# Optimization experiments

Hardware: AMD Instinct MI355X
Metric: run time of the kernel (lower is better)

Reference implementation:

```python
import jax, jax.numpy as jnp
import numpy as np

B, C_ENC, H, W = 8, 512, 96, 96
N_SAMP = 64            # num_samples in forward
N_NODES = 2 * N_SAMP   # 64 pos + 64 neg per image
D = 256                # node feature dim after head_in_ln
N_HEADS = 8
DH = D // N_HEADS
SINKHORN_ITERS = 10


def _ln(x):
    # LayerNorm(elementwise_affine=False)
    m = x.mean(-1, keepdims=True)
    v = x.var(-1, keepdims=True)
    return (x - m) / jnp.sqrt(v + 1e-5)


def setup_inputs() -> dict:
    key = jax.random.key(0)
    ks = jax.random.split(key, 12)
    std = 0.01  # matches nn.init.normal_(std=0.01) in _init_weights
    inp = {
        "feat_s": jax.random.normal(ks[0], (B, C_ENC, H, W), jnp.float32),
        "score_s": jax.random.normal(ks[1], (B, 1, H, W), jnp.float32),
        "feat_t": jax.random.normal(ks[2], (B, C_ENC, H, W), jnp.float32),
        "score_t": jax.random.normal(ks[3], (B, 1, H, W), jnp.float32),
        "head_W1": std * jax.random.normal(ks[4], (C_ENC, D), jnp.float32),
        "head_b1": jnp.zeros((D,), jnp.float32),
        "head_W2": std * jax.random.normal(ks[5], (D, D), jnp.float32),
        "head_b2": jnp.zeros((D,), jnp.float32),
        "intra_W": jax.random.normal(ks[6], (4, D, D), jnp.float32) / jnp.sqrt(jnp.float32(D)),
        "intra_b": jnp.zeros((4, D), jnp.float32),
        "cross_W": jax.random.normal(ks[7], (4, D, D), jnp.float32) / jnp.sqrt(jnp.float32(D)),
        "cross_b": jnp.zeros((4, D), jnp.float32),
        "cls_W1": std * jax.random.normal(ks[8], (D, 128), jnp.float32),
        "cls_b1": jnp.zeros((128,), jnp.float32),
        "cls_W2": std * jax.random.normal(ks[9], (128, 1), jnp.float32),
        "cls_b2": jnp.zeros((1,), jnp.float32),
        "aff_A": jax.random.normal(ks[10], (D, D), jnp.float32) / jnp.sqrt(jnp.float32(D)),
    }
    return inp


def _sample_points(feat, score):
    # torch version: boolean-mask nonzero + random gather of 64 pos / 64 neg spatial
    # locations per image. JIT-friendly deterministic equivalent: top-64 highest
    # sigmoid scores = positives, top-64 lowest = negatives.
    s = jax.nn.sigmoid(score[:, 0].reshape(B, -1))            # [B, H*W]
    _, pos_idx = jax.lax.top_k(s, N_SAMP)
    _, neg_idx = jax.lax.top_k(-s, N_SAMP)
    idx = jnp.concatenate([pos_idx, neg_idx], axis=1)         # [B, 128]
    ff = feat.reshape(B, C_ENC, -1)                           # [B, 512, H*W]
    nodes = jnp.take_along_axis(ff, idx[:, None, :], axis=2)  # [B, 512, 128]
    nodes = nodes.transpose(0, 2, 1)                          # [B, 128, 512]
    labels = jnp.concatenate(
        [jnp.ones((B, N_SAMP, 1), feat.dtype), jnp.zeros((B, N_SAMP, 1), feat.dtype)], axis=1)
    return nodes, labels


def _mha(xq, xkv, Wp, bp):
    # standard multi-head attention (MultiHeadAttentionWrapper)
    q = xq @ Wp[0] + bp[0]
    k = xkv @ Wp[1] + bp[1]
    v = xkv @ Wp[2] + bp[2]
    sh = lambda t: t.reshape(t.shape[0], t.shape[1], N_HEADS, DH)
    att = jnp.einsum("bqhd,bkhd->bhqk", sh(q), sh(k)) / jnp.sqrt(jnp.float32(DH))
    att = jax.nn.softmax(att, axis=-1)
    o = jnp.einsum("bhqk,bkhd->bqhd", att, sh(v)).reshape(xq.shape[0], xq.shape[1], D)
    return o @ Wp[3] + bp[3], att.mean(1)


def _forward(feat_s, score_s, feat_t, score_t, head_W1, head_b1, head_W2, head_b2,
             intra_W, intra_b, cross_W, cross_b, cls_W1, cls_b1, cls_W2, cls_b2, aff_A):
    n1, l1 = _sample_points(feat_s, score_s)
    n2, l2 = _sample_points(feat_t, score_t)

    # head_in_ln: Linear -> LN -> ReLU -> Linear -> LN
    head = lambda x: _ln(jax.nn.relu(_ln(x @ head_W1 + head_b1)) @ head_W2 + head_b2)
    n1, n2 = head(n1), head(n2)

    # intra-domain graph (self-attention), shared weights for both domains
    n1, _ = _mha(n1, n1, intra_W, intra_b)
    n2, _ = _mha(n2, n2, intra_W, intra_b)

    # cross-domain graph (cross-attention both directions, shared weights)
    c1, _ = _mha(n1, n2, cross_W, cross_b)
    c2, _ = _mha(n2, n1, cross_W, cross_b)
    n1, n2 = c1, c2

    # node classification loss (BCEWithLogits, mean)
    cls = lambda x: jax.nn.relu(x @ cls_W1 + cls_b1) @ cls_W2 + cls_b2
    def bce_logits(logit, lab):
        return jnp.mean(jnp.maximum(logit, 0) - logit * lab + jnp.log1p(jnp.exp(-jnp.abs(logit))))
    node_loss = bce_logits(cls(n1), l1) + bce_logits(cls(n2), l2)

    # affinity + InstanceNorm2d(1) + sinkhorn refine
    Mmat = jnp.einsum("bnd,de,bme->bnm", n1, aff_A, n2)       # [B, 128, 128]
    mu = Mmat.mean((1, 2), keepdims=True)
    var = Mmat.var((1, 2), keepdims=True)
    K = (Mmat - mu) / jnp.sqrt(var + 1e-5)
    for _ in range(SINKHORN_ITERS):  # log-space row/col normalization
        K = K - jax.nn.logsumexp(K, axis=2, keepdims=True)
        K = K - jax.nn.logsumexp(K, axis=1, keepdims=True)
    P = jnp.exp(K)

    # matching loss = BCEFocalLoss(gamma=2, alpha=0.25) vs label-agreement matrix
    gt = (l1[:, :, 0][:, :, None] == l2[:, :, 0][:, None, :]).astype(P.dtype)
    pt = jnp.clip(P, 1e-6, 1.0 - 1e-6)
    mat_loss = jnp.mean(-0.25 * (1 - pt) ** 2 * gt * jnp.log(pt)
                        - 0.75 * pt ** 2 * (1 - gt) * jnp.log(1 - pt))

    total_loss = node_loss + 10.0 * mat_loss
    return n1, total_loss


def reference(feat_s, score_s, feat_t, score_t, head_W1, head_b1, head_W2, head_b2,
              intra_W, intra_b, cross_W, cross_b, cls_W1, cls_b1, cls_W2, cls_b2, aff_A):
    return _forward(feat_s, score_s, feat_t, score_t, head_W1, head_b1, head_W2, head_b2,
                    intra_W, intra_b, cross_W, cross_b, cls_W1, cls_b1, cls_W2, cls_b2, aff_A)
```

## Files before the change

### kernel.cpp

```cpp
#include <hip/hip_runtime.h>
#include <math.h>

#define BIMG 8
#define HW 9216
#define CENC 512
#define NN 128
#define DD 256
#define NHEAD 8
#define DH 32
#define ROWS1 1024
#define ROWS2 2048
#define TAILB 520

typedef unsigned long long ull;
typedef unsigned short u16;
typedef __attribute__((ext_vector_type(4))) float f32x4;
typedef __attribute__((ext_vector_type(4))) unsigned u32x4;
typedef __attribute__((ext_vector_type(2))) unsigned u32x2;

__device__ __forceinline__ u16 f2bf(float f) {
  unsigned u = __float_as_uint(f);
  u += 0x7fffu + ((u >> 16) & 1u);
  return (u16)(u >> 16);
}
__device__ __forceinline__ float bf2f(unsigned h) { return __uint_as_float(h << 16); }
__device__ __forceinline__ unsigned pack2(float a, float b) {
  return (unsigned)f2bf(a) | ((unsigned)f2bf(b) << 16);
}
__device__ __forceinline__ void mfma_b(f32x4& acc, u32x4 a, u32x4 b) {
  asm volatile("v_mfma_f32_16x16x32_bf16 %0, %1, %2, %0" : "+v"(acc) : "v"(a), "v"(b));
}

__device__ __forceinline__ ull cmpex_keep(ull k, ull o, bool keepMax) {
  return ((k > o) == keepMax) ? k : o;
}
__device__ __forceinline__ void bsort64(ull& k, int lane) {
#pragma unroll
  for (int size = 2; size <= 64; size <<= 1) {
#pragma unroll
    for (int stride = size >> 1; stride > 0; stride >>= 1) {
      ull o = __shfl_xor(k, stride);
      bool keepMax = (((lane & size) == 0) == ((lane & stride) == 0));
      k = cmpex_keep(k, o, keepMax);
    }
  }
}
__device__ __forceinline__ void bmerge64(ull& top, ull b, int lane) {
  ull rev = __shfl_xor(b, 63);
  ull m = top > rev ? top : rev;
#pragma unroll
  for (int stride = 32; stride > 0; stride >>= 1) {
    ull o = __shfl_xor(m, stride);
    m = cmpex_keep(m, o, (lane & stride) == 0);
  }
  top = m;
}
__device__ __forceinline__ ull lds_merge(ull a, ull brev, int lane) {
  ull m = a > brev ? a : brev;
#pragma unroll
  for (int stride = 32; stride > 0; stride >>= 1) {
    ull o = __shfl_xor(m, stride);
    m = cmpex_keep(m, o, (lane & stride) == 0);
  }
  return m;
}

__global__ __launch_bounds__(512) void head_kernel(const float* __restrict__ score_s,
                                                   const float* __restrict__ score_t,
                                                   int* __restrict__ idx_out,
                                                   float* __restrict__ loss_acc,
                                                   const float* __restrict__ hw1,
                                                   const float* __restrict__ hw2,
                                                   const float* __restrict__ iw,
                                                   const float* __restrict__ cw,
                                                   const float* __restrict__ aw,
                                                   const float* __restrict__ clsW1,
                                                   const float* __restrict__ intra_b,
                                                   const float* __restrict__ cross_b,
                                                   u16* __restrict__ wt,
                                                   u16* __restrict__ w1t,
                                                   u16* __restrict__ wt_f,
                                                   float* __restrict__ bfq) {
  __shared__ union {
    struct { ull sm[512]; float tile[32][33]; } a;
    struct { float Wo[32][264]; float Wc[256][40]; } b;
  } HS;
  int tid = threadIdx.x;
  if (blockIdx.x < 32) {
    int blk = blockIdx.x;
    int bi = blk >> 1, neg = blk & 1;
    int lane = tid & 63, w = tid >> 6;
    if (blk == 0 && tid < 4) loss_acc[tid] = 0.f;
    const float* sp = (bi < 8 ? score_s : score_t) + (size_t)(bi & 7) * HW;
    int q0 = w * 18;
    ull keys[18];
#pragma unroll
    for (int j = 0; j < 18; ++j) {
      float x = sp[(q0 + j) * 64 + lane];
      unsigned ub = __float_as_uint(x);
      unsigned u = (ub & 0x80000000u) ? ~ub : (ub | 0x80000000u);
      if (neg) u = ~u;
      int gi = (q0 + j) * 64 + lane;
      keys[j] = ((ull)u << 32) | (unsigned)(~gi);
    }
    ull top1 = keys[0]; bsort64(top1, lane);
    ull top2 = keys[9]; bsort64(top2, lane);
#pragma unroll
    for (int j = 1; j < 9; ++j) {
      ull k1 = keys[j], k2 = keys[9 + j];
      bsort64(k1, lane);
      bsort64(k2, lane);
      bmerge64(top1, k1, lane);
      bmerge64(top2, k2, lane);
    }
    bmerge64(top1, top2, lane);
    HS.a.sm[w * 64 + lane] = top1;
    __syncthreads();
    if (w < 4) {
      ull m = lds_merge(HS.a.sm[(2 * w) * 64 + lane],
                        HS.a.sm[(2 * w + 1) * 64 + (63 - lane)], lane);
      HS.a.sm[(2 * w) * 64 + lane] = m;
    }
    __syncthreads();
    if (w < 2) {
      ull m = lds_merge(HS.a.sm[(4 * w) * 64 + lane],
                        HS.a.sm[(4 * w + 2) * 64 + (63 - lane)], lane);
      HS.a.sm[(4 * w) * 64 + lane] = m;
    }
    __syncthreads();
    if (w == 0) {
      ull m = lds_merge(HS.a.sm[lane], HS.a.sm[4 * 64 + (63 - lane)], lane);
      idx_out[bi * NN + neg * 64 + lane] = (int)(~(unsigned)(m & 0xffffffffull));
    }
  } else if (blockIdx.x < 800) {
    int bid = blockIdx.x - 32;
    const float* src; u16* dst; int K, k0, n0;
    if (bid < 128) {
      src = hw1; dst = wt; K = 512;
      k0 = (bid >> 3) * 32; n0 = (bid & 7) * 32;
    } else {
      int id2 = bid - 128;
      int m = id2 >> 6, tt = id2 & 63;
      K = 256;
      k0 = (tt >> 3) * 32; n0 = (tt & 7) * 32;
      src = (m == 0) ? hw2 : (m < 5) ? iw + (size_t)(m - 1) * 65536
          : (m < 9) ? cw + (size_t)(m - 5) * 65536 : aw;
      dst = wt + 131072 + (size_t)m * 65536;
    }
    int r = tid >> 3, c = (tid & 7) * 4;
    if (tid < 256) {
      float4 v = *(const float4*)&src[(size_t)(k0 + r) * 256 + n0 + c];
      HS.a.tile[r][c] = v.x; HS.a.tile[r][c + 1] = v.y;
      HS.a.tile[r][c + 2] = v.z; HS.a.tile[r][c + 3] = v.w;
    }
    __syncthreads();
    if (tid < 256) {
      u32x2 o;
      o[0] = pack2(HS.a.tile[c][r], HS.a.tile[c + 1][r]);
      o[1] = pack2(HS.a.tile[c + 2][r], HS.a.tile[c + 3][r]);
      *(u32x2*)&dst[(size_t)(n0 + r) * K + k0 + c] = o;
    }
  } else if (blockIdx.x < 832) {
    int bid3 = blockIdx.x - 800;
    int k0 = (bid3 >> 2) * 32, n0 = (bid3 & 3) * 32;
    int r = tid >> 3, c = (tid & 7) * 4;
    if (tid < 256) {
      float4 v = *(const float4*)&clsW1[(size_t)(k0 + r) * 128 + n0 + c];
      HS.a.tile[r][c] = v.x; HS.a.tile[r][c + 1] = v.y;
      HS.a.tile[r][c + 2] = v.z; HS.a.tile[r][c + 3] = v.w;
    }
    __syncthreads();
    if (tid < 256) {
      u32x2 o;
      o[0] = pack2(HS.a.tile[c][r], HS.a.tile[c + 1][r]);
      o[1] = pack2(HS.a.tile[c + 2][r], HS.a.tile[c + 3][r]);
      *(u32x2*)&w1t[(size_t)(n0 + r) * 256 + k0 + c] = o;
    }
  } else {
    int bid4 = blockIdx.x - 832;
    int z = bid4 >> 6, tt = bid4 & 63;
    int k0 = (tt >> 3) * 32, n0 = (tt & 7) * 32;
    const float* Wo = iw + 3 * 65536;
    const float* Wc = cw + (size_t)z * 65536;
    for (int e = tid; e < 2048; e += 512) {
      int row = e >> 6, c4 = (e & 63) * 4;
      *(float4*)&HS.b.Wo[row][c4] = *(const float4*)&Wo[(size_t)(k0 + row) * 256 + c4];
    }
    for (int e = tid; e < 2048; e += 512) {
      int row = e >> 3, c4 = (e & 7) * 4;
      *(float4*)&HS.b.Wc[row][c4] = *(const float4*)&Wc[(size_t)row * 256 + n0 + c4];
    }
    __syncthreads();
    int k = tid >> 4, half = (tid >> 3) & 1, nb = (tid & 7) * 4;
    float a0 = 0.f, a1 = 0.f, a2 = 0.f, a3 = 0.f;
    int jb = half * 128;
#pragma unroll 8
    for (int j = 0; j < 128; ++j) {
      float wo = HS.b.Wo[k][jb + j];
      float4 wc = *(const float4*)&HS.b.Wc[jb + j][nb];
      a0 += wo * wc.x; a1 += wo * wc.y; a2 += wo * wc.z; a3 += wo * wc.w;
    }
    a0 += __shfl_xor(a0, 8); a1 += __shfl_xor(a1, 8);
    a2 += __shfl_xor(a2, 8); a3 += __shfl_xor(a3, 8);
    if (half == 0) {
      u16* dst = wt_f + (size_t)z * 65536;
      dst[(size_t)(n0 + nb + 0) * 256 + k0 + k] = f2bf(a0);
      dst[(size_t)(n0 + nb + 1) * 256 + k0 + k] = f2bf(a1);
      dst[(size_t)(n0 + nb + 2) * 256 + k0 + k] = f2bf(a2);
      dst[(size_t)(n0 + nb + 3) * 256 + k0 + k] = f2bf(a3);
    }
    if (k0 == 0 && tid < 32) {
      float b = 0.f;
      const float* bo = intra_b + 768;
      for (int j = 0; j < 256; ++j) b += bo[j] * HS.b.Wc[j][tid];
      bfq[z * 256 + n0 + tid] = b + cross_b[z * 256 + n0 + tid];
    }
  }
}

__global__ __launch_bounds__(512) void gemm1_fused(const float* __restrict__ feat_s,
                                                   const float* __restrict__ feat_t,
                                                   const int* __restrict__ idxb,
                                                   const u16* __restrict__ wt_h1,
                                                   const float* __restrict__ head_b1,
                                                   u16* __restrict__ bufA,
                                                   float* __restrict__ st1) {
  __shared__ u16 As[16][520];
  __shared__ u16 Bs[256][40];
  int t = threadIdx.x, l = t & 63, w = t >> 6;
  int m0 = blockIdx.x * 16;
#pragma unroll
  for (int row = 0; row < 16; ++row) {
    int grow = m0 + row;
    int bi = grow >> 7, n = grow & 127, b = bi & 7;
    const float* fp = (bi < 8) ? feat_s : feat_t;
    int pos = idxb[bi * NN + n];
    As[row][t] = f2bf(fp[(size_t)b * CENC * HW + (size_t)t * HW + pos]);
  }
  __syncthreads();
  f32x4 acc[2];
  acc[0] = (f32x4){0.f, 0.f, 0.f, 0.f};
  acc[1] = (f32x4){0.f, 0.f, 0.f, 0.f};
  for (int kc = 0; kc < 16; ++kc) {
#pragma unroll
    for (int i = 0; i < 2; ++i) {
      int e = t + i * 512;
      int nn2 = e >> 2, ch8 = (e & 3) * 8;
      *(u32x4*)&Bs[nn2][ch8] = *(const u32x4*)&wt_h1[(size_t)nn2 * 512 + kc * 32 + ch8];
    }
    __syncthreads();
    u32x4 af = *(const u32x4*)&As[l & 15][kc * 32 + (l >> 4) * 8];
#pragma unroll
    for (int i = 0; i < 2; ++i) {
      u32x4 bf = *(const u32x4*)&Bs[w * 32 + i * 16 + (l & 15)][(l >> 4) * 8];
      mfma_b(acc[i], af, bf);
    }
    __syncthreads();
  }
  asm volatile("s_nop 7\n\ts_nop 7" ::);
  int rbase = m0 + (l >> 4) * 4;
#pragma unroll
  for (int i = 0; i < 2; ++i) {
    int col = w * 32 + i * 16 + (l & 15);
    float bb = head_b1[col];
#pragma unroll
    for (int r = 0; r < 4; ++r) {
      int row = rbase + r;
      float o = acc[i][r] + bb;
      bufA[(size_t)row * 256 + col] = f2bf(o);
      float s = o, q = o * o;
#pragma unroll
      for (int m = 1; m < 16; m <<= 1) { s += __shfl_xor(s, m); q += __shfl_xor(q, m); }
      if ((l & 15) == 0) {
        st1[(size_t)row * 32 + w * 2 + i]      = s;
        st1[(size_t)row * 32 + 16 + w * 2 + i] = q;
      }
    }
  }
}

template<int K>
__global__ __launch_bounds__(512) void gemm_mf(const u16* __restrict__ A,
                                               const u16* __restrict__ Wt,
                                               const float* __restrict__ bias,
                                               u16* __restrict__ Cb,
                                               float* __restrict__ Cf,
                                               int ldc,
                                               const float* __restrict__ in_stats, int in_relu,
                                               float* __restrict__ out_stats,
                                               int Wz, int Cbz, int bz) {
  constexpr int LDK = K + 8;
  constexpr int KC = K / 8;
  __shared__ u16 As[32][LDK];
  __shared__ u16 Bs[64][LDK];
  __shared__ float mS[32], rS[32];
  int z = blockIdx.z;
  Wt += (size_t)z * Wz;
  if (Cb)   Cb += (size_t)z * Cbz;
  if (bias) bias += (size_t)z * bz;
  int n0 = blockIdx.x * 64, m0 = blockIdx.y * 32;
  int t = threadIdx.x;
  if (in_stats) {
    if (t < 32) {
      const float* sp = in_stats + (size_t)(m0 + t) * 32;
      float s = 0.f, q = 0.f;
#pragma unroll
      for (int i = 0; i < 16; ++i) { s += sp[i]; q += sp[16 + i]; }
      float mm = s * (1.f / 256.f);
      float var = q * (1.f / 256.f) - mm * mm;
      mS[t] = mm;
      rS[t] = rsqrtf(fmaxf(var, 0.f) + 1e-5f);
    }
    __syncthreads();
  }
  for (int i = t; i < 32 * KC; i += 512) {
    int row = i / KC, c8 = (i % KC) * 8;
    u32x4 av = *(const u32x4*)&A[(size_t)(m0 + row) * K + c8];
    if (in_stats) {
      float mm = mS[row], rr = rS[row];
#pragma unroll
      for (int j = 0; j < 4; ++j) {
        float f0 = (bf2f(av[j] & 0xffffu) - mm) * rr;
        float f1 = (bf2f(av[j] >> 16) - mm) * rr;
        if (in_relu) { f0 = fmaxf(f0, 0.f); f1 = fmaxf(f1, 0.f); }
        av[j] = pack2(f0, f1);
      }
    }
    *(u32x4*)&As[row][c8] = av;
  }
  for (int i = t; i < 64 * KC; i += 512) {
    int row = i / KC, c8 = (i % KC) * 8;
    *(u32x4*)&Bs[row][c8] = *(const u32x4*)&Wt[(size_t)(n0 + row) * K + c8];
  }
  __syncthreads();
  int l = t & 63, w = t >> 6;
  int wr = w >> 2, wc = w & 3;
  int fra = wr * 16 + (l & 15);
  int frk = (l >> 4) * 8;
  int fb = wc * 16 + (l & 15);
  f32x4 acc = {0.f, 0.f, 0.f, 0.f};
#pragma unroll
  for (int ks = 0; ks < K / 32; ++ks) {
    u32x4 af = *(const u32x4*)&As[fra][ks * 32 + frk];
    u32x4 bf = *(const u32x4*)&Bs[fb][ks * 32 + frk];
    mfma_b(acc, af, bf);
  }
  asm volatile("s_nop 7\n\ts_nop 7" ::);
  int col0 = n0 + wc * 16 + (l & 15);
  int rbase = m0 + wr * 16 + (l >> 4) * 4;
  float b0 = bias ? bias[col0] : 0.f;
#pragma unroll
  for (int r = 0; r < 4; ++r) {
    int row = rbase + r;
    float o0 = acc[r] + b0;
    if (Cb) Cb[(size_t)row * 256 + col0] = f2bf(o0);
    if (Cf && row < ROWS1) Cf[(size_t)row * ldc + col0] = o0;
    if (out_stats) {
      float s0 = o0, q0 = o0 * o0;
#pragma unroll
      for (int m = 1; m < 16; m <<= 1) { s0 += __shfl_xor(s0, m); q0 += __shfl_xor(q0, m); }
      if ((l & 15) == 0) {
        int slot = (n0 >> 4) + wc;
        out_stats[(size_t)row * 32 + slot]      = s0;
        out_stats[(size_t)row * 32 + 16 + slot] = q0;
      }
    }
  }
}

__global__ __launch_bounds__(256) void attn_kernel(const u16* __restrict__ q,
                                                   const u16* __restrict__ k,
                                                   const u16* __restrict__ v,
                                                   u16* __restrict__ o, int swap) {
  __shared__ __align__(16) float Ks[NN][DH];
  __shared__ __align__(16) float Vs[NN][DH];
  __shared__ __align__(16) float Ex[64][3][34];
  int blk = blockIdx.x;
  int bb = blk >> 4, h = (blk >> 1) & 7, qh = blk & 1;
  int kb = swap ? (bb ^ 8) : bb;
  int t = threadIdx.x;
  int rr = t & 63, part = t >> 6;
  for (int e = t; e < 1024; e += 256) {
    int which = e >> 9;
    int idx2 = e & 511;
    int r = idx2 >> 2, c8 = (idx2 & 3) * 8;
    u32x4 val = *(const u32x4*)&(which ? v : k)[(size_t)(kb * NN + r) * DD + h * DH + c8];
    float* dst = which ? &Vs[r][c8] : &Ks[r][c8];
#pragma unroll
    for (int i = 0; i < 4; ++i) {
      dst[2 * i]     = bf2f(val[i] & 0xffffu);
      dst[2 * i + 1] = bf2f(val[i] >> 16);
    }
  }
  __syncthreads();
  int qrow = bb * NN + qh * 64 + rr;
  float4 q4[8];
  {
    const u16* qp = q + (size_t)qrow * DD + h * DH;
#pragma unroll
    for (int c4 = 0; c4 < 4; ++c4) {
      u32x4 u = *(const u32x4*)&qp[c4 * 8];
      q4[c4 * 2].x = bf2f(u[0] & 0xffffu); q4[c4 * 2].y = bf2f(u[0] >> 16);
      q4[c4 * 2].z = bf2f(u[1] & 0xffffu); q4[c4 * 2].w = bf2f(u[1] >> 16);
      q4[c4 * 2 + 1].x = bf2f(u[2] & 0xffffu); q4[c4 * 2 + 1].y = bf2f(u[2] >> 16);
      q4[c4 * 2 + 1].z = bf2f(u[3] & 0xffffu); q4[c4 * 2 + 1].w = bf2f(u[3] >> 16);
    }
  }
  const float scale = 0.17677669529663687f;
  int j0 = part * 32;
  float mx = -1e30f;
  for (int j = j0; j < j0 + 32; ++j) {
    const float4* kp = (const float4*)Ks[j];
    float s = 0.f;
#pragma unroll
    for (int c4 = 0; c4 < 8; ++c4) {
      float4 kv = kp[c4];
      s += q4[c4].x * kv.x + q4[c4].y * kv.y + q4[c4].z * kv.z + q4[c4].w * kv.w;
    }
    mx = fmaxf(mx, s * scale);
  }
  float acc[DH];
#pragma unroll
  for (int c = 0; c < DH; ++c) acc[c] = 0.f;
  float den = 0.f;
  for (int j = j0; j < j0 + 32; ++j) {
    const float4* kp = (const float4*)Ks[j];
    float s = 0.f;
#pragma unroll
    for (int c4 = 0; c4 < 8; ++c4) {
      float4 kv = kp[c4];
      s += q4[c4].x * kv.x + q4[c4].y * kv.y + q4[c4].z * kv.z + q4[c4].w * kv.w;
    }
    float e = __expf(s * scale - mx);
    den += e;
    const float4* vp = (const float4*)Vs[j];
#pragma unroll
    for (int c4 = 0; c4 < 8; ++c4) {
      float4 vv = vp[c4];
      acc[c4 * 4 + 0] += e * vv.x; acc[c4 * 4 + 1] += e * vv.y;
      acc[c4 * 4 + 2] += e * vv.z; acc[c4 * 4 + 3] += e * vv.w;
    }
  }
  if (part) {
#pragma unroll
    for (int c = 0; c < DH; ++c) Ex[rr][part - 1][c] = acc[c];
    Ex[rr][part - 1][32] = mx;
    Ex[rr][part - 1][33] = den;
  }
  __syncthreads();
  if (part == 0) {
    float M = mx;
#pragma unroll
    for (int p = 0; p < 3; ++p) M = fmaxf(M, Ex[rr][p][32]);
    float f0 = __expf(mx - M);
    float fp[3];
    float dt = den * f0;
#pragma unroll
    for (int p = 0; p < 3; ++p) { fp[p] = __expf(Ex[rr][p][32] - M); dt += Ex[rr][p][33] * fp[p]; }
    float inv = 1.0f / dt;
    unsigned ovu[16];
#pragma unroll
    for (int c = 0; c < 16; ++c) {
      float x0 = acc[2 * c] * f0, x1 = acc[2 * c + 1] * f0;
#pragma unroll
      for (int p = 0; p < 3; ++p) { x0 += Ex[rr][p][2 * c] * fp[p]; x1 += Ex[rr][p][2 * c + 1] * fp[p]; }
      ovu[c] = pack2(x0 * inv, x1 * inv);
    }
    unsigned* op = (unsigned*)(o + (size_t)qrow * DD + h * DH);
#pragma unroll
    for (int i = 0; i < 4; ++i) {
      u32x4 w4;
      w4[0] = ovu[4 * i]; w4[1] = ovu[4 * i + 1]; w4[2] = ovu[4 * i + 2]; w4[3] = ovu[4 * i + 3];
      *(u32x4*)&op[4 * i] = w4;
    }
  }
}

struct SkSmem {
  union { u16 tmpL[128][264]; float Km[128][133]; } u;
  float u_[NN];
  float v_[NN];
  float red[20];
};
struct ClsSmem {
  float xs[4][256];
  float part[4][128];
  float red[8];
};
union TailSmem { SkSmem sk; ClsSmem cls; };

__device__ __forceinline__ void ticket_finalize(float* acc, float* out) {
  __threadfence();
  int tk = atomicAdd((int*)acc + 3, 1);
  if (tk == TAILB - 1) {
    float a0 = atomicAdd(acc + 0, 0.0f);
    float a1 = atomicAdd(acc + 1, 0.0f);
    out[ROWS1 * DD] = a0 + 10.0f * a1;
  }
}

__global__ __launch_bounds__(1024) void tail_kernel(const u16* __restrict__ bufH,
                                                    const u16* __restrict__ wt_af,
                                                    const u16* __restrict__ w1t,
                                                    const float* __restrict__ b1,
                                                    const float* __restrict__ W2,
                                                    const float* __restrict__ b2,
                                                    float* __restrict__ acc,
                                                    float* __restrict__ out) {
  __shared__ TailSmem sm;
  int t = threadIdx.x;
  int bid = blockIdx.x;
  if (bid < 8) {
    int b = bid;
    int l = t & 63, w = t >> 6;
    int tr = w >> 1;
    const u16* c1 = bufH + (size_t)(b * 128) * 256;
    const u16* c2 = bufH + (size_t)(1024 + b * 128) * 256;
    {
      int tcB = (w & 1) * 8;
      f32x4 accA[8];
#pragma unroll
      for (int i = 0; i < 8; ++i) accA[i] = (f32x4){0.f, 0.f, 0.f, 0.f};
      for (int ks = 0; ks < 8; ++ks) {
        int kk = ks * 32 + (l >> 4) * 8;
        u32x4 af = *(const u32x4*)&c1[(size_t)(tr * 16 + (l & 15)) * 256 + kk];
#pragma unroll
        for (int i = 0; i < 8; ++i) {
          u32x4 bf = *(const u32x4*)&wt_af[(size_t)((tcB + i) * 16 + (l & 15)) * 256 + kk];
          mfma_b(accA[i], af, bf);
        }
      }
      asm volatile("s_nop 7\n\ts_nop 7" ::);
      int rb = tr * 16 + (l >> 4) * 4;
#pragma unroll
      for (int i = 0; i < 8; ++i) {
        int col = (tcB + i) * 16 + (l & 15);
#pragma unroll
        for (int r2 = 0; r2 < 4; ++r2)
          sm.sk.u.tmpL[rb + r2][col] = f2bf(accA[i][r2]);
      }
    }
    __syncthreads();
    f32x4 aB[4];
    {
      int tcB = (w & 1) * 4;
#pragma unroll
      for (int i = 0; i < 4; ++i) aB[i] = (f32x4){0.f, 0.f, 0.f, 0.f};
      for (int ks = 0; ks < 8; ++ks) {
        int kk = ks * 32 + (l >> 4) * 8;
        u32x4 af = *(const u32x4*)&sm.sk.u.tmpL[tr * 16 + (l & 15)][kk];
#pragma unroll
        for (int i = 0; i < 4; ++i) {
          u32x4 bf = *(const u32x4*)&c2[(size_t)((tcB + i) * 16 + (l & 15)) * 256 + kk];
          mfma_b(aB[i], af, bf);
        }
      }
      asm volatile("s_nop 7\n\ts_nop 7" ::);
    }
    __syncthreads();
    {
      int tcB = (w & 1) * 4;
      int rb = tr * 16 + (l >> 4) * 4;
#pragma unroll
      for (int i = 0; i < 4; ++i) {
        int col = (tcB + i) * 16 + (l & 15);
#pragma unroll
        for (int r2 = 0; r2 < 4; ++r2)
          sm.sk.u.Km[rb + r2][col] = aB[i][r2];
      }
    }
    __syncthreads();
    int r = t >> 3, cg = t & 7;
    int c = t >> 3, rg = t & 7;
    float kr[16], kc[16];
    {
#pragma unroll
      for (int q4 = 0; q4 < 4; ++q4) {
        float4 f = *(const float4*)&sm.sk.u.Km[r][cg * 16 + q4 * 4];
        kr[q4 * 4 + 0] = f.x; kr[q4 * 4 + 1] = f.y; kr[q4 * 4 + 2] = f.z; kr[q4 * 4 + 3] = f.w;
      }
#pragma unroll
      for (int q = 0; q < 16; ++q)
        kc[q] = sm.sk.u.Km[rg * 16 + q][c];
    }
    float s = 0.f;
#pragma unroll
    for (int q = 0; q < 16; ++q) s += kr[q];
    for (int m = 1; m < 64; m <<= 1) s += __shfl_xor(s, m);
    if ((t & 63) == 0) sm.sk.red[t >> 6] = s;
    __syncthreads();
    if (t == 0) { float tt = 0.f; for (int i = 0; i < 16; ++i) tt += sm.sk.red[i]; sm.sk.red[16] = tt; }
    __syncthreads();
    float mu = sm.sk.red[16] * (1.0f / 16384.f);
    __syncthreads();
    float sq = 0.f;
#pragma unroll
    for (int q = 0; q < 16; ++q) { float d = kr[q] - mu; sq += d * d; }
    for (int m = 1; m < 64; m <<= 1) sq += __shfl_xor(sq, m);
    if ((t & 63) == 0) sm.sk.red[t >> 6] = sq;
    __syncthreads();
    if (t == 0) { float tt = 0.f; for (int i = 0; i < 16; ++i) tt += sm.sk.red[i]; sm.sk.red[17] = tt; }
    __syncthreads();
    float inv = 1.0f / sqrtf(sm.sk.red[17] * (1.0f / 16384.f) + 1e-5f);
#pragma unroll
    for (int q = 0; q < 16; ++q) { kr[q] = (kr[q] - mu) * inv; kc[q] = (kc[q] - mu) * inv; }
    if (t < NN) { sm.sk.u_[t] = 0.f; sm.sk.v_[t] = 0.f; }
    __syncthreads();
    for (int iter = 0; iter < 10; ++iter) {
      float tmp[16];
      {
        const float4* vp = (const float4*)(sm.sk.v_ + cg * 16);
#pragma unroll
        for (int q4 = 0; q4 < 4; ++q4) {
          float4 f = vp[q4];
          tmp[q4 * 4 + 0] = kr[q4 * 4 + 0] - f.x; tmp[q4 * 4 + 1] = kr[q4 * 4 + 1] - f.y;
          tmp[q4 * 4 + 2] = kr[q4 * 4 + 2] - f.z; tmp[q4 * 4 + 3] = kr[q4 * 4 + 3] - f.w;
        }
        float mx = tmp[0];
#pragma unroll
        for (int q = 1; q < 16; ++q) mx = fmaxf(mx, tmp[q]);
        for (int m = 1; m < 8; m <<= 1) mx = fmaxf(mx, __shfl_xor(mx, m));
        float smv = 0.f;
#pragma unroll
        for (int q = 0; q < 16; ++q) smv += __expf(tmp[q] - mx);
        for (int m = 1; m < 8; m <<= 1) smv += __shfl_xor(smv, m);
        if (cg == 0) sm.sk.u_[r] = mx + __logf(smv);
      }
      __syncthreads();
      {
        const float4* up = (const float4*)(sm.sk.u_ + rg * 16);
#pragma unroll
        for (int q4 = 0; q4 < 4; ++q4) {
          float4 f = up[q4];
          tmp[q4 * 4 + 0] = kc[q4 * 4 + 0] - f.x; tmp[q4 * 4 + 1] = kc[q4 * 4 + 1] - f.y;
          tmp[q4 * 4 + 2] = kc[q4 * 4 + 2] - f.z; tmp[q4 * 4 + 3] = kc[q4 * 4 + 3] - f.w;
        }
        float mx = tmp[0];
#pragma unroll
        for (int q = 1; q < 16; ++q) mx = fmaxf(mx, tmp[q]);
        for (int m = 1; m < 8; m <<= 1) mx = fmaxf(mx, __shfl_xor(mx, m));
        float smv = 0.f;
#pragma unroll
        for (int q = 0; q < 16; ++q) smv += __expf(tmp[q] - mx);
        for (int m = 1; m < 8; m <<= 1) smv += __shfl_xor(smv, m);
        if (rg == 0) sm.sk.v_[c] = mx + __logf(smv);
      }
      __syncthreads();
    }
    float ur = sm.sk.u_[r];
    float fsum = 0.f;
    {
      const float4* vp = (const float4*)(sm.sk.v_ + cg * 16);
#pragma unroll
      for (int q4 = 0; q4 < 4; ++q4) {
        float4 f = vp[q4];
        float vv[4] = {f.x, f.y, f.z, f.w};
#pragma unroll
        for (int j = 0; j < 4; ++j) {
          float P = __expf(kr[q4 * 4 + j] - ur - vv[j]);
          float pt = fminf(fmaxf(P, 1e-6f), 1.0f - 1e-6f);
          int col = cg * 16 + q4 * 4 + j;
          bool gt = (r < 64) == (col < 64);
          float wgt = gt ? (-0.25f * (1.f - pt) * (1.f - pt)) : (-0.75f * pt * pt);
          float lg = gt ? __logf(pt) : __logf(1.f - pt);
          fsum += wgt * lg;
        }
      }
    }
    for (int m = 1; m < 64; m <<= 1) fsum += __shfl_xor(fsum, m);
    if ((t & 63) == 0) sm.sk.red[t >> 6] = fsum;
    __syncthreads();
    if (t == 0) {
      float tt = 0.f; for (int i = 0; i < 16; ++i) tt += sm.sk.red[i];
      atomicAdd(acc + 1, tt * (1.0f / 131072.f));
      ticket_finalize(acc, out);
    }
  } else {
    int row0 = (bid - 8) * 4;
    {
      int rr = t >> 8, cc = t & 255;
      sm.cls.xs[rr][cc] = bf2f(bufH[(size_t)(row0 + rr) * 256 + cc]);
    }
    __syncthreads();
    int grp = t >> 8, col = t & 127, kh = (t >> 7) & 1;
    const u16* wp = w1t + (size_t)col * 256 + kh * 128;
    const float* xp = &sm.cls.xs[grp][kh * 128];
    float h = 0.f;
#pragma unroll
    for (int i = 0; i < 16; ++i) {
      u32x4 wv = *(const u32x4*)&wp[i * 8];
      const float* x8 = xp + i * 8;
      h += x8[0] * bf2f(wv[0] & 0xffffu) + x8[1] * bf2f(wv[0] >> 16)
         + x8[2] * bf2f(wv[1] & 0xffffu) + x8[3] * bf2f(wv[1] >> 16)
         + x8[4] * bf2f(wv[2] & 0xffffu) + x8[5] * bf2f(wv[2] >> 16)
         + x8[6] * bf2f(wv[3] & 0xffffu) + x8[7] * bf2f(wv[3] >> 16);
    }
    if (kh == 1) sm.cls.part[grp][col] = h;
    __syncthreads();
    if (kh == 0) {
      float z = h + sm.cls.part[grp][col] + b1[col];
      float p = fmaxf(z, 0.f) * W2[col];
#pragma unroll
      for (int m = 1; m < 64; m <<= 1) p += __shfl_xor(p, m);
      if ((t & 63) == 0) sm.cls.red[grp * 2 + ((t >> 6) & 1)] = p;
    }
    __syncthreads();
    if (t == 0) {
      float total = 0.f;
      float bb2 = b2[0];
#pragma unroll
      for (int g = 0; g < 4; ++g) {
        float z = sm.cls.red[2 * g] + sm.cls.red[2 * g + 1] + bb2;
        float lab = (((row0 + g) & 127) < 64) ? 1.f : 0.f;
        total += fmaxf(z, 0.f) - z * lab + log1pf(__expf(-fabsf(z)));
      }
      atomicAdd(acc, total * (1.0f / 1024.0f));
      ticket_finalize(acc, out);
    }
  }
}

extern "C" void kernel_launch(void* const* d_in, const int* in_sizes, int n_in,
                              void* d_out, int out_size, void* d_ws, size_t ws_size,
                              hipStream_t stream) {
  const float* feat_s  = (const float*)d_in[0];
  const float* score_s = (const float*)d_in[1];
  const float* feat_t  = (const float*)d_in[2];
  const float* score_t = (const float*)d_in[3];
  const float* head_W1 = (const float*)d_in[4];
  const float* head_b1 = (const float*)d_in[5];
  const float* head_W2 = (const float*)d_in[6];
  const float* head_b2 = (const float*)d_in[7];
  const float* intra_W = (const float*)d_in[8];
  const float* intra_b = (const float*)d_in[9];
  const float* cross_W = (const float*)d_in[10];
  const float* cross_b = (const float*)d_in[11];
  const float* cls_W1  = (const float*)d_in[12];
  const float* cls_b1  = (const float*)d_in[13];
  const float* cls_W2  = (const float*)d_in[14];
  const float* cls_b2  = (const float*)d_in[15];
  const float* aff_A   = (const float*)d_in[16];

  u16* bufA  = (u16*)d_ws;
  u16* bufB  = bufA + ROWS2 * DD;
  u16* bufH  = bufB + ROWS2 * DD;
  u16* qkv   = bufH + ROWS2 * DD;
  u16* attnb = qkv + 3 * ROWS2 * DD;
  u16* wt    = attnb + ROWS2 * DD;
  u16* w1t   = wt + 786432;
  u16* wt_f  = w1t + 32768;
  float* st1 = (float*)(wt_f + 3 * 65536);
  float* st2 = st1 + ROWS2 * 32;
  float* bfq = st2 + ROWS2 * 32;
  float* acc = bfq + 768;
  int* idxb  = (int*)(acc + 8);
  float* out_f = (float*)d_out;

  u16* wt_h1 = wt;
  u16* wt_h2 = wt + 131072;
  u16* wt_in = wt_h2 + 65536;
  u16* wt_cr = wt_in + 4 * 65536;
  u16* wt_af = wt_cr + 4 * 65536;

  head_kernel<<<1024, 512, 0, stream>>>(score_s, score_t, idxb, acc,
                                        head_W1, head_W2, intra_W, cross_W, aff_A, cls_W1,
                                        intra_b, cross_b, wt, w1t, wt_f, bfq);
  gemm1_fused<<<128, 512, 0, stream>>>(feat_s, feat_t, idxb, wt_h1, head_b1, bufA, st1);

  dim3 g1(4, 64, 1);
  dim3 gq(4, 64, 3);
  const float* nulf = nullptr;
  float* nulw = nullptr;

  gemm_mf<256><<<g1, 512, 0, stream>>>(bufA, wt_h2, head_b2, bufB, nulw, 0, st1, 1, st2,
                                       0, 0, 0);
  gemm_mf<256><<<gq, 512, 0, stream>>>(bufB, wt_in, intra_b, qkv, nulw, 0, st2, 0, nulw,
                                       65536, ROWS2 * DD, 256);
  attn_kernel<<<256, 256, 0, stream>>>(qkv, qkv + ROWS2 * DD, qkv + 2 * ROWS2 * DD,
                                       attnb, 0);
  gemm_mf<256><<<gq, 512, 0, stream>>>(attnb, wt_f, bfq, qkv, nulw, 0, nulf, 0, nulw,
                                       65536, ROWS2 * DD, 256);
  attn_kernel<<<256, 256, 0, stream>>>(qkv, qkv + ROWS2 * DD, qkv + 2 * ROWS2 * DD,
                                       attnb, 1);
  gemm_mf<256><<<g1, 512, 0, stream>>>(attnb, wt_cr + 3 * 65536, cross_b + 768, bufH, out_f,
                                       256, nulf, 0, nulw, 0, 0, 0);
  tail_kernel<<<TAILB, 1024, 0, stream>>>(bufH, wt_af, w1t, cls_b1, cls_W2, cls_b2,
                                          acc, out_f);
}
```

Measured before the change: 207.5 us.

## Fuse QKV projection GEMM with attention into per-head MFMA kernel

Replaces the separate batched QKV projection GEMM and the scalar-FP32 attention kernel with one kernel per (image, head). It projects Q/K/V for that head with MFMA, then computes QK^T and P·V with MFMA in shared memory, applying LayerNorm from precomputed stats inline. This removes two kernel launches and the qkv round trip through global memory, and moves the attention math onto matrix cores. In exchange, each block recomputes its K/V projection inputs, uses large shared memory with only 128 blocks, and rounds P to bf16.

```diff
diff --git a/kernel.cpp b/kernel.cpp
--- a/kernel.cpp
+++ b/kernel.cpp
@@ -29,6 +29,9 @@
 }
 __device__ __forceinline__ void mfma_b(f32x4& acc, u32x4 a, u32x4 b) {
   asm volatile("v_mfma_f32_16x16x32_bf16 %0, %1, %2, %0" : "+v"(acc) : "v"(a), "v"(b));
+}
+__device__ __forceinline__ void mfma_s(f32x4& acc, u32x4 a, u32x4 b) {
+  asm volatile("s_nop 1\n\tv_mfma_f32_16x16x32_bf16 %0, %1, %2, %0" : "+v"(acc) : "v"(a), "v"(b));
 }
 
 __device__ __forceinline__ ull cmpex_keep(ull k, ull o, bool keepMax) {
@@ -287,17 +290,12 @@
                                                float* __restrict__ Cf,
                                                int ldc,
                                                const float* __restrict__ in_stats, int in_relu,
-                                               float* __restrict__ out_stats,
-                                               int Wz, int Cbz, int bz) {
+                                               float* __restrict__ out_stats) {
   constexpr int LDK = K + 8;
   constexpr int KC = K / 8;
   __shared__ u16 As[32][LDK];
   __shared__ u16 Bs[64][LDK];
   __shared__ float mS[32], rS[32];
-  int z = blockIdx.z;
-  Wt += (size_t)z * Wz;
-  if (Cb)   Cb += (size_t)z * Cbz;
-  if (bias) bias += (size_t)z * bz;
   int n0 = blockIdx.x * 64, m0 = blockIdx.y * 32;
   int t = threadIdx.x;
   if (in_stats) {
@@ -368,110 +366,123 @@
   }
 }
 
-__global__ __launch_bounds__(256) void attn_kernel(const u16* __restrict__ q,
-                                                   const u16* __restrict__ k,
-                                                   const u16* __restrict__ v,
-                                                   u16* __restrict__ o, int swap) {
-  __shared__ __align__(16) float Ks[NN][DH];
-  __shared__ __align__(16) float Vs[NN][DH];
-  __shared__ __align__(16) float Ex[64][3][34];
+template<int HASLN, int SWAP>
+__global__ __launch_bounds__(1024) void fattn_kernel(const u16* __restrict__ X,
+                                                     const u16* __restrict__ Wt,
+                                                     const float* __restrict__ bias,
+                                                     const float* __restrict__ stats,
+                                                     u16* __restrict__ O) {
+  __shared__ u16 Qs[128][40];
+  __shared__ u16 Ks[128][40];
+  __shared__ u16 Vt[32][136];
+  __shared__ float Sf[128][132];
+  __shared__ u16 Pb[128][136];
+  __shared__ float mS[128], rS[128], dn[128];
   int blk = blockIdx.x;
-  int bb = blk >> 4, h = (blk >> 1) & 7, qh = blk & 1;
-  int kb = swap ? (bb ^ 8) : bb;
-  int t = threadIdx.x;
-  int rr = t & 63, part = t >> 6;
-  for (int e = t; e < 1024; e += 256) {
-    int which = e >> 9;
-    int idx2 = e & 511;
-    int r = idx2 >> 2, c8 = (idx2 & 3) * 8;
-    u32x4 val = *(const u32x4*)&(which ? v : k)[(size_t)(kb * NN + r) * DD + h * DH + c8];
-    float* dst = which ? &Vs[r][c8] : &Ks[r][c8];
-#pragma unroll
-    for (int i = 0; i < 4; ++i) {
-      dst[2 * i]     = bf2f(val[i] & 0xffffu);
-      dst[2 * i + 1] = bf2f(val[i] >> 16);
+  int bb = blk >> 3, h = blk & 7;
+  int kb = SWAP ? (bb ^ 8) : bb;
+  int baseQ = bb * 128, baseKV = kb * 128;
+  int t = threadIdx.x, l = t & 63, w = t >> 6;
+  if (HASLN) {
+    if (t < 128) {
+      const float* sp = stats + (size_t)(baseQ + t) * 32;
+      float s = 0.f, q = 0.f;
+#pragma unroll
+      for (int i = 0; i < 16; ++i) { s += sp[i]; q += sp[16 + i]; }
+      float mm = s * (1.f / 256.f);
+      mS[t] = mm;
+      rS[t] = rsqrtf(fmaxf(q * (1.f / 256.f) - mm * mm, 0.f) + 1e-5f);
+    }
+    __syncthreads();
+  }
+  const float scale = 0.17677669529663687f;
+  int mt = w >> 1, nt = w & 1;
+#pragma unroll
+  for (int z = 0; z < 3; ++z) {
+    const u16* Xz = X + (size_t)(z == 0 ? baseQ : baseKV) * 256;
+    f32x4 acc = {0.f, 0.f, 0.f, 0.f};
+    int ar = mt * 16 + (l & 15);
+    int bn = h * 32 + nt * 16 + (l & 15);
+#pragma unroll
+    for (int ks = 0; ks < 8; ++ks) {
+      int ak = ks * 32 + (l >> 4) * 8;
+      u32x4 af = *(const u32x4*)&Xz[(size_t)ar * 256 + ak];
+      if (HASLN) {
+        float mm = mS[ar], rr = rS[ar];
+#pragma unroll
+        for (int j = 0; j < 4; ++j) {
+          float f0 = (bf2f(af[j] & 0xffffu) - mm) * rr;
+          float f1 = (bf2f(af[j] >> 16) - mm) * rr;
+          af[j] = pack2(f0, f1);
+        }
+      }
+      u32x4 bf = *(const u32x4*)&Wt[(size_t)z * 65536 + (size_t)bn * 256 + ak];
+      mfma_s(acc, af, bf);
+    }
+    asm volatile("s_nop 7\n\ts_nop 7" ::);
+    float bv = bias[z * 256 + h * 32 + nt * 16 + (l & 15)];
+    int cn = nt * 16 + (l & 15);
+#pragma unroll
+    for (int r2 = 0; r2 < 4; ++r2) {
+      int rr2 = mt * 16 + (l >> 4) * 4 + r2;
+      float v = acc[r2] + bv;
+      if (z == 0)      Qs[rr2][cn] = f2bf(v);
+      else if (z == 1) Ks[rr2][cn] = f2bf(v);
+      else             Vt[cn][rr2] = f2bf(v);
     }
   }
   __syncthreads();
-  int qrow = bb * NN + qh * 64 + rr;
-  float4 q4[8];
+#pragma unroll
+  for (int i = 0; i < 4; ++i) {
+    int tile = w * 4 + i, mt2 = tile >> 3, nt2 = tile & 7;
+    f32x4 acc = {0.f, 0.f, 0.f, 0.f};
+    u32x4 af = *(const u32x4*)&Qs[mt2 * 16 + (l & 15)][(l >> 4) * 8];
+    u32x4 bf = *(const u32x4*)&Ks[nt2 * 16 + (l & 15)][(l >> 4) * 8];
+    mfma_s(acc, af, bf);
+    asm volatile("s_nop 7\n\ts_nop 7" ::);
+#pragma unroll
+    for (int r2 = 0; r2 < 4; ++r2)
+      Sf[mt2 * 16 + (l >> 4) * 4 + r2][nt2 * 16 + (l & 15)] = acc[r2] * scale;
+  }
+  __syncthreads();
   {
-    const u16* qp = q + (size_t)qrow * DD + h * DH;
-#pragma unroll
-    for (int c4 = 0; c4 < 4; ++c4) {
-      u32x4 u = *(const u32x4*)&qp[c4 * 8];
-      q4[c4 * 2].x = bf2f(u[0] & 0xffffu); q4[c4 * 2].y = bf2f(u[0] >> 16);
-      q4[c4 * 2].z = bf2f(u[1] & 0xffffu); q4[c4 * 2].w = bf2f(u[1] >> 16);
-      q4[c4 * 2 + 1].x = bf2f(u[2] & 0xffffu); q4[c4 * 2 + 1].y = bf2f(u[2] >> 16);
-      q4[c4 * 2 + 1].z = bf2f(u[3] & 0xffffu); q4[c4 * 2 + 1].w = bf2f(u[3] >> 16);
-    }
-  }
-  const float scale = 0.17677669529663687f;
-  int j0 = part * 32;
-  float mx = -1e30f;
-  for (int j = j0; j < j0 + 32; ++j) {
-    const float4* kp = (const float4*)Ks[j];
-    float s = 0.f;
-#pragma unroll
-    for (int c4 = 0; c4 < 8; ++c4) {
-      float4 kv = kp[c4];
-      s += q4[c4].x * kv.x + q4[c4].y * kv.y + q4[c4].z * kv.z + q4[c4].w * kv.w;
-    }
-    mx = fmaxf(mx, s * scale);
-  }
-  float acc[DH];
-#pragma unroll
-  for (int c = 0; c < DH; ++c) acc[c] = 0.f;
-  float den = 0.f;
-  for (int j = j0; j < j0 + 32; ++j) {
-    const float4* kp = (const float4*)Ks[j];
-    float s = 0.f;
-#pragma unroll
-    for (int c4 = 0; c4 < 8; ++c4) {
-      float4 kv = kp[c4];
-      s += q4[c4].x * kv.x + q4[c4].y * kv.y + q4[c4].z * kv.z + q4[c4].w * kv.w;
-    }
-    float e = __expf(s * scale - mx);
-    den += e;
-    const float4* vp = (const float4*)Vs[j];
-#pragma unroll
-    for (int c4 = 0; c4 < 8; ++c4) {
-      float4 vv = vp[c4];
-      acc[c4 * 4 + 0] += e * vv.x; acc[c4 * 4 + 1] += e * vv.y;
-      acc[c4 * 4 + 2] += e * vv.z; acc[c4 * 4 + 3] += e * vv.w;
-    }
-  }
-  if (part) {
-#pragma unroll
-    for (int c = 0; c < DH; ++c) Ex[rr][part - 1][c] = acc[c];
-    Ex[rr][part - 1][32] = mx;
-    Ex[rr][part - 1][33] = den;
+    int r = t >> 3, p = t & 7;
+    int js = p * 16;
+    float v[16];
+#pragma unroll
+    for (int q4 = 0; q4 < 4; ++q4) {
+      float4 f = *(const float4*)&Sf[r][js + q4 * 4];
+      v[q4 * 4 + 0] = f.x; v[q4 * 4 + 1] = f.y; v[q4 * 4 + 2] = f.z; v[q4 * 4 + 3] = f.w;
+    }
+    float mx = v[0];
+#pragma unroll
+    for (int j = 1; j < 16; ++j) mx = fmaxf(mx, v[j]);
+    for (int m = 1; m < 8; m <<= 1) mx = fmaxf(mx, __shfl_xor(mx, m));
+    float e[16];
+    float den = 0.f;
+#pragma unroll
+    for (int j = 0; j < 16; ++j) { e[j] = __expf(v[j] - mx); den += e[j]; }
+    for (int m = 1; m < 8; m <<= 1) den += __shfl_xor(den, m);
+    unsigned* pw = (unsigned*)&Pb[r][js];
+#pragma unroll
+    for (int jp = 0; jp < 8; ++jp) pw[jp] = pack2(e[2 * jp], e[2 * jp + 1]);
+    if (p == 0) dn[r] = 1.0f / den;
   }
   __syncthreads();
-  if (part == 0) {
-    float M = mx;
-#pragma unroll
-    for (int p = 0; p < 3; ++p) M = fmaxf(M, Ex[rr][p][32]);
-    float f0 = __expf(mx - M);
-    float fp[3];
-    float dt = den * f0;
-#pragma unroll
-    for (int p = 0; p < 3; ++p) { fp[p] = __expf(Ex[rr][p][32] - M); dt += Ex[rr][p][33] * fp[p]; }
-    float inv = 1.0f / dt;
-    unsigned ovu[16];
-#pragma unroll
-    for (int c = 0; c < 16; ++c) {
-      float x0 = acc[2 * c] * f0, x1 = acc[2 * c + 1] * f0;
-#pragma unroll
-      for (int p = 0; p < 3; ++p) { x0 += Ex[rr][p][2 * c] * fp[p]; x1 += Ex[rr][p][2 * c + 1] * fp[p]; }
-      ovu[c] = pack2(x0 * inv, x1 * inv);
-    }
-    unsigned* op = (unsigned*)(o + (size_t)qrow * DD + h * DH);
-#pragma unroll
-    for (int i = 0; i < 4; ++i) {
-      u32x4 w4;
-      w4[0] = ovu[4 * i]; w4[1] = ovu[4 * i + 1]; w4[2] = ovu[4 * i + 2]; w4[3] = ovu[4 * i + 3];
-      *(u32x4*)&op[4 * i] = w4;
+  {
+    f32x4 acc = {0.f, 0.f, 0.f, 0.f};
+#pragma unroll
+    for (int ks = 0; ks < 4; ++ks) {
+      u32x4 af = *(const u32x4*)&Pb[mt * 16 + (l & 15)][ks * 32 + (l >> 4) * 8];
+      u32x4 bf = *(const u32x4*)&Vt[nt * 16 + (l & 15)][ks * 32 + (l >> 4) * 8];
+      mfma_s(acc, af, bf);
+    }
+    asm volatile("s_nop 7\n\ts_nop 7" ::);
+    int cn = nt * 16 + (l & 15);
+#pragma unroll
+    for (int r2 = 0; r2 < 4; ++r2) {
+      int rr2 = mt * 16 + (l >> 4) * 4 + r2;
+      O[(size_t)(baseQ + rr2) * 256 + h * 32 + cn] = f2bf(acc[r2] * dn[rr2]);
     }
   }
 }
@@ -548,11 +559,11 @@
       for (int i = 0; i < 4; ++i) aB[i] = (f32x4){0.f, 0.f, 0.f, 0.f};
       for (int ks = 0; ks < 8; ++ks) {
         int kk = ks * 32 + (l >> 4) * 8;
-        u32x4 af = *(const u32x4*)&sm.sk.u.tmpL[tr * 16 + (l & 15)][kk];
+        u32x4 a0 = *(const u32x4*)&sm.sk.u.tmpL[tr * 16 + (l & 15)][kk];
 #pragma unroll
         for (int i = 0; i < 4; ++i) {
           u32x4 bf = *(const u32x4*)&c2[(size_t)((tcB + i) * 16 + (l & 15)) * 256 + kk];
-          mfma_b(aB[i], af, bf);
+          mfma_b(aB[i], a0, bf);
         }
       }
       asm volatile("s_nop 7\n\ts_nop 7" ::);
@@ -744,9 +755,9 @@
   u16* bufA  = (u16*)d_ws;
   u16* bufB  = bufA + ROWS2 * DD;
   u16* bufH  = bufB + ROWS2 * DD;
-  u16* qkv   = bufH + ROWS2 * DD;
-  u16* attnb = qkv + 3 * ROWS2 * DD;
-  u16* wt    = attnb + ROWS2 * DD;
+  u16* attnb = bufH + ROWS2 * DD;
+  u16* atto2 = attnb + ROWS2 * DD;
+  u16* wt    = atto2 + ROWS2 * DD;
   u16* w1t   = wt + 786432;
   u16* wt_f  = w1t + 32768;
   float* st1 = (float*)(wt_f + 3 * 65536);
@@ -768,22 +779,14 @@
   gemm1_fused<<<128, 512, 0, stream>>>(feat_s, feat_t, idxb, wt_h1, head_b1, bufA, st1);
 
   dim3 g1(4, 64, 1);
-  dim3 gq(4, 64, 3);
   const float* nulf = nullptr;
   float* nulw = nullptr;
 
-  gemm_mf<256><<<g1, 512, 0, stream>>>(bufA, wt_h2, head_b2, bufB, nulw, 0, st1, 1, st2,
-                                       0, 0, 0);
-  gemm_mf<256><<<gq, 512, 0, stream>>>(bufB, wt_in, intra_b, qkv, nulw, 0, st2, 0, nulw,
-                                       65536, ROWS2 * DD, 256);
-  attn_kernel<<<256, 256, 0, stream>>>(qkv, qkv + ROWS2 * DD, qkv + 2 * ROWS2 * DD,
-                                       attnb, 0);
-  gemm_mf<256><<<gq, 512, 0, stream>>>(attnb, wt_f, bfq, qkv, nulw, 0, nulf, 0, nulw,
-                                       65536, ROWS2 * DD, 256);
-  attn_kernel<<<256, 256, 0, stream>>>(qkv, qkv + ROWS2 * DD, qkv + 2 * ROWS2 * DD,
-                                       attnb, 1);
-  gemm_mf<256><<<g1, 512, 0, stream>>>(attnb, wt_cr + 3 * 65536, cross_b + 768, bufH, out_f,
-                                       256, nulf, 0, nulw, 0, 0, 0);
+  gemm_mf<256><<<g1, 512, 0, stream>>>(bufA, wt_h2, head_b2, bufB, nulw, 0, st1, 1, st2);
+  fattn_kernel<1, 0><<<128, 1024, 0, stream>>>(bufB, wt_in, intra_b, st2, attnb);
+  fattn_kernel<0, 1><<<128, 1024, 0, stream>>>(attnb, wt_f, bfq, nulf, atto2);
+  gemm_mf<256><<<g1, 512, 0, stream>>>(atto2, wt_cr + 3 * 65536, cross_b + 768, bufH, out_f,
+                                       256, nulf, 0, nulw);
   tail_kernel<<<TAILB, 1024, 0, stream>>>(bufH, wt_af, w1t, cls_b1, cls_W2, cls_b2,
                                           acc, out_f);
 }
```

Measured after the change: 207.4 us. About the same (-0.1%).
